# Performance work log

Hardware: AMD Instinct MI355X
Metric: run time of the kernel (lower is better)

## Reference

```python
import jax, jax.numpy as jnp
import numpy as np

BN_EPS = 1e-5
NEG_SLOPE = 0.2


def _knn_idx(x, k):
    # x: [B, C, N] -> idx: [B, N, k] of nearest neighbors (incl. self)
    xx = jnp.sum(x * x, axis=1)                      # [B, N]
    inner = jnp.einsum('bcn,bcm->bnm', x, x)          # [B, N, N]
    neg_d2 = -(xx[:, :, None] - 2.0 * inner + xx[:, None, :])
    _, idx = jax.lax.top_k(neg_d2, k)                 # largest -neg dist = nearest
    return idx


def _graph_feature(x, k):
    # x: [B, C, N] -> [B, 2C, N, k] with concat([x_j - x_i, x_i])
    idx = _knn_idx(x, k)                              # [B, N, k]
    xt = jnp.transpose(x, (0, 2, 1))                  # [B, N, C]
    neigh = jax.vmap(lambda xb, ib: xb[ib])(xt, idx)  # [B, N, k, C]
    center = xt[:, :, None, :]                        # [B, N, 1, C]
    feat = jnp.concatenate(
        [neigh - center, jnp.broadcast_to(center, neigh.shape)], axis=-1
    )                                                 # [B, N, k, 2C]
    return jnp.transpose(feat, (0, 3, 1, 2))          # [B, 2C, N, k]


def _edge_conv(x, W, gamma, beta, k):
    # EdgeConv block: graph feature -> 1x1 conv -> BN (train stats) -> LeakyReLU
    f = _graph_feature(x, k)                          # [B, 2C, N, k]
    y = jnp.einsum('oc,bcnk->bonk', W, f)             # 1x1 conv, no bias
    m = jnp.mean(y, axis=(0, 2, 3), keepdims=True)
    v = jnp.mean((y - m) ** 2, axis=(0, 2, 3), keepdims=True)
    y = (y - m) * jax.lax.rsqrt(v + BN_EPS)
    y = y * gamma.reshape(1, -1, 1, 1) + beta.reshape(1, -1, 1, 1)
    return jnp.where(y >= 0, y, NEG_SLOPE * y)


def setup_inputs() -> dict:
    key = jax.random.key(0)
    ks = jax.random.split(key, 8)
    B, Cin, N, K = 16, 4, 1024, 20
    channels = [64, 64, 128, 256]
    in_cs = [2 * Cin, 2 * channels[0], 2 * channels[1], 2 * channels[2]]
    inp = {'x': jax.random.normal(ks[0], (B, 1, Cin, N), dtype=jnp.float32)}
    for i in range(4):
        fan_in = in_cs[i]  # kaiming-ish scale
        inp[f'W{i}'] = jax.random.normal(ks[i + 1], (channels[i], in_cs[i]), dtype=jnp.float32) / np.sqrt(fan_in)
        inp[f'g{i}'] = jnp.ones((channels[i],), dtype=jnp.float32)
        inp[f'b{i}'] = jnp.zeros((channels[i],), dtype=jnp.float32)
    inp['k'] = K
    return inp


def reference(x, W0, g0, b0, W1, g1, b1, W2, g2, b2, W3, g3, b3, k):
    h = jnp.squeeze(x, axis=1)                        # [B, Cin, N]
    params = [(W0, g0, b0), (W1, g1, b1), (W2, g2, b2), (W3, g3, b3)]
    n_layers = len(params)
    for i, (W, g, b) in enumerate(params):
        h = _edge_conv(h, W, g, b, k)                 # [B, C_out, N, k]
        if i < n_layers - 1:
            h = jnp.max(h, axis=-1)                   # max over neighbors -> [B, C_out, N]
    # AdaptiveMaxPool2d((1,1)) over [B, C, N, k]
    return jnp.max(h, axis=(2, 3), keepdims=True)     # [B, C_last, 1, 1]
```

## Files before the change

kernel.cpp:

```cpp
#include <hip/hip_runtime.h>
#include <math.h>

static constexpr int B_ = 16;
static constexpr int N_ = 1024;
static constexpr int K_ = 20;

template<int C>
__global__ __launch_bounds__(256) void xx_kernel(const float* __restrict__ h,
                                                 float* __restrict__ xx) {
  int i = blockIdx.x * 256 + threadIdx.x;
  if (i >= B_ * N_) return;
  int b = i >> 10, n = i & 1023;
  const float* hb = h + (size_t)b * C * N_ + n;
  float s = 0.f;
  #pragma unroll 4
  for (int c = 0; c < C; ++c) { float v = hb[(size_t)c * N_]; s = fmaf(v, v, s); }
  xx[i] = s;
}

template<int C>
__global__ __launch_bounds__(256) void knn_kernel(const float* __restrict__ h,
                                                  const float* __restrict__ xx,
                                                  int* __restrict__ idxg) {
  constexpr int CC = (C < 64) ? C : 64;
  __shared__ float xm_s[CC][128];
  __shared__ float xn_s[C][16];
  const int b  = blockIdx.y;
  const int n0 = blockIdx.x * 16;
  const int tid = threadIdx.x;
  const int lane = tid & 63;
  const int wv   = tid >> 6;
  const int rb   = wv * 4;
  const float* hb = h + (size_t)b * C * N_;
  const float* xxb = xx + b * N_;

  for (int i = tid; i < C * 16; i += 256) {
    int c = i >> 4, r = i & 15;
    xn_s[c][r] = hb[(size_t)c * N_ + n0 + r];
  }
  float xxn[4];
  #pragma unroll
  for (int rr = 0; rr < 4; ++rr) xxn[rr] = xxb[n0 + rb + rr];

  float val[4][16];
  #pragma unroll
  for (int ch = 0; ch < 8; ++ch) {
    const int m0 = ch * 128;
    float acc0[4] = {0.f, 0.f, 0.f, 0.f};
    float acc1[4] = {0.f, 0.f, 0.f, 0.f};
    #pragma unroll
    for (int cc0 = 0; cc0 < C; cc0 += CC) {
      __syncthreads();
      #pragma unroll 4
      for (int i = tid; i < CC * 128; i += 256) {
        int c = i >> 7, mm = i & 127;
        xm_s[c][mm] = hb[(size_t)(cc0 + c) * N_ + m0 + mm];
      }
      __syncthreads();
      #pragma unroll 4
      for (int c = 0; c < CC; ++c) {
        float2 xm2 = *(const float2*)&xm_s[c][2 * lane];
        float4 xn4 = *(const float4*)&xn_s[cc0 + c][rb];
        float xnv[4] = {xn4.x, xn4.y, xn4.z, xn4.w};
        #pragma unroll
        for (int rr = 0; rr < 4; ++rr) {
          acc0[rr] = fmaf(xnv[rr], xm2.x, acc0[rr]);
          acc1[rr] = fmaf(xnv[rr], xm2.y, acc1[rr]);
        }
      }
    }
    float2 xxm2 = *(const float2*)&xxb[m0 + 2 * lane];
    #pragma unroll
    for (int rr = 0; rr < 4; ++rr) {
      val[rr][2 * ch]     = -(fmaf(-2.f, acc0[rr], xxn[rr]) + xxm2.x);
      val[rr][2 * ch + 1] = -(fmaf(-2.f, acc1[rr], xxn[rr]) + xxm2.y);
    }
  }

  #pragma unroll
  for (int pr = 0; pr < 2; ++pr) {
    float (&va)[16] = val[2 * pr];
    float (&vb)[16] = val[2 * pr + 1];
    unsigned colA[16], colB[16];
    #pragma unroll
    for (int t = 0; t < 16; ++t) {
      unsigned col = (unsigned)((t >> 1) * 128 + 2 * lane + (t & 1));
      colA[t] = col; colB[t] = col;
    }
    #pragma unroll
    for (int k = 2; k <= 16; k <<= 1) {
      #pragma unroll
      for (int j = k >> 1; j > 0; j >>= 1) {
        #pragma unroll
        for (int i = 0; i < 16; ++i) {
          int l = i ^ j;
          if (l > i) {
            bool up = (i & k) == 0;
            {
              bool gt = (va[l] > va[i]) || (va[l] == va[i] && colA[l] < colA[i]);
              bool cnd = up ? gt : !gt;
              float tv = va[i]; unsigned tc = colA[i];
              va[i] = cnd ? va[l] : tv;   colA[i] = cnd ? colA[l] : tc;
              va[l] = cnd ? tv : va[l];   colA[l] = cnd ? tc : colA[l];
            }
            {
              bool gt = (vb[l] > vb[i]) || (vb[l] == vb[i] && colB[l] < colB[i]);
              bool cnd = up ? gt : !gt;
              float tv = vb[i]; unsigned tc = colB[i];
              vb[i] = cnd ? vb[l] : tv;   colB[i] = cnd ? colB[l] : tc;
              vb[l] = cnd ? tv : vb[l];   colB[l] = cnd ? tc : colB[l];
            }
          }
        }
      }
    }
    const int outA = (b * N_ + n0 + rb + 2 * pr) * K_;
    const int outB = outA + K_;
    #pragma unroll 1
    for (int it = 0; it < K_; ++it) {
      float bvA = va[0]; unsigned bcA = colA[0];
      float bvB = vb[0]; unsigned bcB = colB[0];
      #pragma unroll
      for (int off = 32; off >= 1; off >>= 1) {
        float ovA = __shfl_xor(bvA, off); unsigned ocA = (unsigned)__shfl_xor((int)bcA, off);
        float ovB = __shfl_xor(bvB, off); unsigned ocB = (unsigned)__shfl_xor((int)bcB, off);
        bool tA = (ovA > bvA) || (ovA == bvA && ocA < bcA);
        bvA = tA ? ovA : bvA; bcA = tA ? ocA : bcA;
        bool tB = (ovB > bvB) || (ovB == bvB && ocB < bcB);
        bvB = tB ? ovB : bvB; bcB = tB ? ocB : bcB;
      }
      if (lane == 0) {
        idxg[outA + it] = (int)bcA;
        idxg[outB + it] = (int)bcB;
      }
      if (colA[0] == bcA) {
        #pragma unroll
        for (int t = 0; t < 15; ++t) { va[t] = va[t + 1]; colA[t] = colA[t + 1]; }
        va[15] = -3.4e38f; colA[15] = 0xFFFFFFFFu;
      }
      if (colB[0] == bcB) {
        #pragma unroll
        for (int t = 0; t < 15; ++t) { vb[t] = vb[t + 1]; colB[t] = colB[t + 1]; }
        vb[15] = -3.4e38f; colB[15] = 0xFFFFFFFFu;
      }
    }
  }
}

template<int C, int CO>
__global__ __launch_bounds__(256) void gemm_uw_kernel(const float* __restrict__ h,
    const float* __restrict__ W, float* __restrict__ ubuf, float* __restrict__ wbuf) {
  __shared__ float hs[C][128];
  __shared__ float Ws[64][C + 1];
  const int b  = blockIdx.z;
  const int n0 = blockIdx.x * 128;
  const int which = blockIdx.y & 1;
  const int o0 = (blockIdx.y >> 1) * 64;
  const int tid = threadIdx.x;
  for (int i = tid; i < 64 * C; i += 256) {
    int o = i / C, c = i % C;
    const float* wr = W + (size_t)(o0 + o) * (2 * C);
    float w1 = wr[c];
    Ws[o][c] = which ? (wr[C + c] - w1) : w1;
  }
  const float* hb = h + (size_t)b * C * N_ + n0;
  for (int i = tid; i < C * 128; i += 256) {
    int c = i >> 7, nn = i & 127;
    hs[c][nn] = hb[(size_t)c * N_ + nn];
  }
  __syncthreads();
  const int ob = (tid & 15) * 4;
  const int nb = (tid >> 4) * 8;
  float acc[8][4];
  #pragma unroll
  for (int i = 0; i < 8; ++i)
    #pragma unroll
    for (int j = 0; j < 4; ++j) acc[i][j] = 0.f;
  for (int c = 0; c < C; ++c) {
    float hv[8];
    *(float4*)&hv[0] = *(const float4*)&hs[c][nb];
    *(float4*)&hv[4] = *(const float4*)&hs[c][nb + 4];
    float w0 = Ws[ob][c], w1 = Ws[ob + 1][c], w2 = Ws[ob + 2][c], w3 = Ws[ob + 3][c];
    #pragma unroll
    for (int i = 0; i < 8; ++i) {
      acc[i][0] = fmaf(hv[i], w0, acc[i][0]);
      acc[i][1] = fmaf(hv[i], w1, acc[i][1]);
      acc[i][2] = fmaf(hv[i], w2, acc[i][2]);
      acc[i][3] = fmaf(hv[i], w3, acc[i][3]);
    }
  }
  float* out = (which ? wbuf : ubuf) + ((size_t)(b * N_ + n0 + nb)) * CO + o0 + ob;
  #pragma unroll
  for (int i = 0; i < 8; ++i) {
    float4 v4; v4.x = acc[i][0]; v4.y = acc[i][1]; v4.z = acc[i][2]; v4.w = acc[i][3];
    *(float4*)(out + (size_t)i * CO) = v4;
  }
}

template<int CO, int NSPLIT>
__global__ __launch_bounds__(256) void passA_kernel(const float* __restrict__ ubuf,
    const float* __restrict__ wbuf, const int* __restrict__ idxg,
    float* __restrict__ Mx, float* __restrict__ Mn, double* __restrict__ stats) {
  __shared__ float us[N_][32];
  const int b = blockIdx.y;
  const int otile = blockIdx.x / NSPLIT;
  const int ns    = blockIdx.x % NSPLIT;
  const int o0 = otile * 32;
  constexpr int NSUB = N_ / NSPLIT;
  const int nstart = ns * NSUB;
  const int tid = threadIdx.x;
  const float* ub = ubuf + (size_t)b * N_ * CO + o0;
  for (int i = tid; i < N_ * 32; i += 256) {
    int n = i >> 5, o = i & 31;
    us[n][o] = ub[(size_t)n * CO + o];
  }
  __syncthreads();
  const int o = tid & 31, ng = tid >> 5;
  double s_y = 0.0, s_y2 = 0.0;
  const size_t bnc = (size_t)b * N_ * CO;
  for (int n = nstart + ng; n < nstart + NSUB; n += 8) {
    const int* ip = idxg + (size_t)(b * N_ + n) * K_;
    int js[20];
    #pragma unroll
    for (int q = 0; q < 5; ++q) {
      int4 t4 = ((const int4*)ip)[q];
      js[q * 4 + 0] = t4.x; js[q * 4 + 1] = t4.y;
      js[q * 4 + 2] = t4.z; js[q * 4 + 3] = t4.w;
    }
    float mx = -3.4e38f, mn = 3.4e38f, s1 = 0.f, s2 = 0.f;
    #pragma unroll
    for (int k = 0; k < 20; ++k) {
      float v = us[js[k]][o];
      mx = fmaxf(mx, v); mn = fminf(mn, v);
      s1 += v; s2 = fmaf(v, v, s2);
    }
    float wvv = wbuf[bnc + (size_t)n * CO + o0 + o];
    s_y  += (double)s1 + 20.0 * (double)wvv;
    s_y2 += (double)s2 + 2.0 * (double)wvv * (double)s1 + 20.0 * (double)wvv * (double)wvv;
    Mx[bnc + (size_t)n * CO + o0 + o] = mx;
    Mn[bnc + (size_t)n * CO + o0 + o] = mn;
  }
  __syncthreads();
  double* sc = (double*)&us[0][0];
  sc[(o * 8 + ng) * 2]     = s_y;
  sc[(o * 8 + ng) * 2 + 1] = s_y2;
  __syncthreads();
  if (tid < 32) {
    double a = 0.0, c2 = 0.0;
    #pragma unroll
    for (int g = 0; g < 8; ++g) { a += sc[(tid * 8 + g) * 2]; c2 += sc[(tid * 8 + g) * 2 + 1]; }
    atomicAdd(&stats[(o0 + tid) * 2],     a);
    atomicAdd(&stats[(o0 + tid) * 2 + 1], c2);
  }
}

template<int CO>
__global__ __launch_bounds__(256) void passB_kernel(const float* __restrict__ Mx,
    const float* __restrict__ Mn, const float* __restrict__ wbuf,
    const double* __restrict__ stats, const float* __restrict__ gam,
    const float* __restrict__ bet, float* __restrict__ hout) {
  __shared__ float T[CO][65];
  __shared__ float a_s[CO], c_s[CO];
  const int b = blockIdx.y, n0 = blockIdx.x * 64;
  const int tid = threadIdx.x;
  const double CNT = (double)B_ * N_ * K_;
  for (int oo = tid; oo < CO; oo += 256) {
    double m  = stats[oo * 2] / CNT;
    double vv = stats[oo * 2 + 1] / CNT - m * m;
    float a = gam[oo] * rsqrtf((float)vv + 1e-5f);
    a_s[oo] = a;
    c_s[oo] = bet[oo] - a * (float)m;
  }
  __syncthreads();
  const size_t base = (size_t)(b * N_ + n0) * CO;
  for (int i = tid; i < 64 * CO; i += 256) {
    int nn = i / CO, oo = i % CO;
    float a = a_s[oo];
    size_t off = base + (size_t)nn * CO + oo;
    float selv = (a >= 0.f) ? Mx[off] : Mn[off];
    float z = fmaf(a, selv + wbuf[off], c_s[oo]);
    T[oo][nn] = (z >= 0.f) ? z : 0.2f * z;
  }
  __syncthreads();
  float* hb = hout + (size_t)b * CO * N_ + n0;
  for (int i = tid; i < 64 * CO; i += 256) {
    int oo = i >> 6, nn = i & 63;
    hb[(size_t)oo * N_ + nn] = T[oo][nn];
  }
}

__global__ __launch_bounds__(256) void final_kernel(const float* __restrict__ Mx,
    const float* __restrict__ Mn, const float* __restrict__ wbuf,
    const double* __restrict__ stats, const float* __restrict__ gam,
    const float* __restrict__ bet, float* __restrict__ out) {
  const int b = blockIdx.x, o = threadIdx.x;
  const double CNT = (double)B_ * N_ * K_;
  double m  = stats[o * 2] / CNT;
  double vv = stats[o * 2 + 1] / CNT - m * m;
  float a = gam[o] * rsqrtf((float)vv + 1e-5f);
  float c = bet[o] - a * (float)m;
  const float* mp = ((a >= 0.f) ? Mx : Mn) + (size_t)b * N_ * 256 + o;
  const float* wp = wbuf + (size_t)b * N_ * 256 + o;
  float best = -3.4e38f;
  for (int n = 0; n < N_; ++n) {
    float z = fmaf(a, mp[(size_t)n * 256] + wp[(size_t)n * 256], c);
    z = (z >= 0.f) ? z : 0.2f * z;
    best = fmaxf(best, z);
  }
  out[b * 256 + o] = best;
}

__global__ void zero_stats(double* p) {
  int i = blockIdx.x * 256 + threadIdx.x;
  if (i < 2048) p[i] = 0.0;
}

extern "C" void kernel_launch(void* const* d_in, const int* in_sizes, int n_in,
                              void* d_out, int out_size, void* d_ws, size_t ws_size,
                              hipStream_t stream) {
  (void)in_sizes; (void)n_in; (void)out_size; (void)ws_size;
  const float* x  = (const float*)d_in[0];
  const float* W0 = (const float*)d_in[1];
  const float* g0 = (const float*)d_in[2];
  const float* b0 = (const float*)d_in[3];
  const float* W1 = (const float*)d_in[4];
  const float* g1 = (const float*)d_in[5];
  const float* b1 = (const float*)d_in[6];
  const float* W2 = (const float*)d_in[7];
  const float* g2 = (const float*)d_in[8];
  const float* b2 = (const float*)d_in[9];
  const float* W3 = (const float*)d_in[10];
  const float* g3 = (const float*)d_in[11];
  const float* b3 = (const float*)d_in[12];

  float* ws  = (float*)d_ws;
  float* u   = ws;
  float* w   = u  + (size_t)B_ * N_ * 256;
  float* Mx  = w  + (size_t)B_ * N_ * 256;
  float* Mn  = Mx + (size_t)B_ * N_ * 256;
  float* h0b = Mn + (size_t)B_ * N_ * 256;
  float* h1b = h0b + (size_t)B_ * 128 * N_;
  float* xxv = h1b + (size_t)B_ * 128 * N_;
  int*   idx = (int*)(xxv + B_ * N_);
  double* stats = (double*)(idx + (size_t)B_ * N_ * K_);

  zero_stats<<<8, 256, 0, stream>>>(stats);

  xx_kernel<4><<<B_ * N_ / 256, 256, 0, stream>>>(x, xxv);
  knn_kernel<4><<<dim3(64, B_), 256, 0, stream>>>(x, xxv, idx);
  gemm_uw_kernel<4, 64><<<dim3(8, 2, B_), 256, 0, stream>>>(x, W0, u, w);
  passA_kernel<64, 8><<<dim3(16, B_), 256, 0, stream>>>(u, w, idx, Mx, Mn, stats);
  passB_kernel<64><<<dim3(16, B_), 256, 0, stream>>>(Mx, Mn, w, stats, g0, b0, h0b);

  xx_kernel<64><<<B_ * N_ / 256, 256, 0, stream>>>(h0b, xxv);
  knn_kernel<64><<<dim3(64, B_), 256, 0, stream>>>(h0b, xxv, idx);
  gemm_uw_kernel<64, 64><<<dim3(8, 2, B_), 256, 0, stream>>>(h0b, W1, u, w);
  passA_kernel<64, 8><<<dim3(16, B_), 256, 0, stream>>>(u, w, idx, Mx, Mn, stats + 512);
  passB_kernel<64><<<dim3(16, B_), 256, 0, stream>>>(Mx, Mn, w, stats + 512, g1, b1, h1b);

  xx_kernel<64><<<B_ * N_ / 256, 256, 0, stream>>>(h1b, xxv);
  knn_kernel<64><<<dim3(64, B_), 256, 0, stream>>>(h1b, xxv, idx);
  gemm_uw_kernel<64, 128><<<dim3(8, 4, B_), 256, 0, stream>>>(h1b, W2, u, w);
  passA_kernel<128, 4><<<dim3(16, B_), 256, 0, stream>>>(u, w, idx, Mx, Mn, stats + 1024);
  passB_kernel<128><<<dim3(16, B_), 256, 0, stream>>>(Mx, Mn, w, stats + 1024, g2, b2, h0b);

  xx_kernel<128><<<B_ * N_ / 256, 256, 0, stream>>>(h0b, xxv);
  knn_kernel<128><<<dim3(64, B_), 256, 0, stream>>>(h0b, xxv, idx);
  gemm_uw_kernel<128, 256><<<dim3(8, 8, B_), 256, 0, stream>>>(h0b, W3, u, w);
  passA_kernel<256, 2><<<dim3(16, B_), 256, 0, stream>>>(u, w, idx, Mx, Mn, stats + 1536);
  final_kernel<<<B_, 256, 0, stream>>>(Mx, Mn, w, stats + 1536, g3, b3, (float*)d_out);
}
```

Baseline: 1.457 ms.

## Extract top-2 per wave reduction round in kNN selection, processing all four rows together

The kNN top-k extraction now merges the two best candidates per lane in each butterfly shuffle round, giving two neighbors per round and halving the number of wave-wide reductions (10 instead of 20). The four rows' sorted lists are handled in one loop instead of two pairs, which interleaves more independent shuffle chains. In exchange, each round costs more shuffles and compares, list shifts become branchless double shifts, and all four rows' value and column arrays stay live at once, which raises register pressure.

```diff
diff --git a/kernel.cpp b/kernel.cpp
--- a/kernel.cpp
+++ b/kernel.cpp
@@ -77,16 +77,12 @@
     }
   }
 
-  #pragma unroll
-  for (int pr = 0; pr < 2; ++pr) {
-    float (&va)[16] = val[2 * pr];
-    float (&vb)[16] = val[2 * pr + 1];
-    unsigned colA[16], colB[16];
-    #pragma unroll
-    for (int t = 0; t < 16; ++t) {
-      unsigned col = (unsigned)((t >> 1) * 128 + 2 * lane + (t & 1));
-      colA[t] = col; colB[t] = col;
-    }
+  unsigned col_[4][16];
+  #pragma unroll
+  for (int r = 0; r < 4; ++r) {
+    #pragma unroll
+    for (int t = 0; t < 16; ++t)
+      col_[r][t] = (unsigned)((t >> 1) * 128 + 2 * lane + (t & 1));
     #pragma unroll
     for (int k = 2; k <= 16; k <<= 1) {
       #pragma unroll
@@ -96,52 +92,60 @@
           int l = i ^ j;
           if (l > i) {
             bool up = (i & k) == 0;
-            {
-              bool gt = (va[l] > va[i]) || (va[l] == va[i] && colA[l] < colA[i]);
-              bool cnd = up ? gt : !gt;
-              float tv = va[i]; unsigned tc = colA[i];
-              va[i] = cnd ? va[l] : tv;   colA[i] = cnd ? colA[l] : tc;
-              va[l] = cnd ? tv : va[l];   colA[l] = cnd ? tc : colA[l];
-            }
-            {
-              bool gt = (vb[l] > vb[i]) || (vb[l] == vb[i] && colB[l] < colB[i]);
-              bool cnd = up ? gt : !gt;
-              float tv = vb[i]; unsigned tc = colB[i];
-              vb[i] = cnd ? vb[l] : tv;   colB[i] = cnd ? colB[l] : tc;
-              vb[l] = cnd ? tv : vb[l];   colB[l] = cnd ? tc : colB[l];
-            }
+            bool gt = (val[r][l] > val[r][i]) ||
+                      (val[r][l] == val[r][i] && col_[r][l] < col_[r][i]);
+            bool cnd = up ? gt : !gt;
+            float tv = val[r][i]; unsigned tc = col_[r][i];
+            val[r][i] = cnd ? val[r][l] : tv;   col_[r][i] = cnd ? col_[r][l] : tc;
+            val[r][l] = cnd ? tv : val[r][l];   col_[r][l] = cnd ? tc : col_[r][l];
           }
         }
       }
     }
-    const int outA = (b * N_ + n0 + rb + 2 * pr) * K_;
-    const int outB = outA + K_;
-    #pragma unroll 1
-    for (int it = 0; it < K_; ++it) {
-      float bvA = va[0]; unsigned bcA = colA[0];
-      float bvB = vb[0]; unsigned bcB = colB[0];
+  }
+
+  const int outbase = (b * N_ + n0 + rb) * K_;
+  #pragma unroll 1
+  for (int it = 0; it < K_ / 2; ++it) {
+    #pragma unroll
+    for (int r = 0; r < 4; ++r) {
+      float    a0v = val[r][0], a1v = val[r][1];
+      unsigned a0c = col_[r][0], a1c = col_[r][1];
       #pragma unroll
       for (int off = 32; off >= 1; off >>= 1) {
-        float ovA = __shfl_xor(bvA, off); unsigned ocA = (unsigned)__shfl_xor((int)bcA, off);
-        float ovB = __shfl_xor(bvB, off); unsigned ocB = (unsigned)__shfl_xor((int)bcB, off);
-        bool tA = (ovA > bvA) || (ovA == bvA && ocA < bcA);
-        bvA = tA ? ovA : bvA; bcA = tA ? ocA : bcA;
-        bool tB = (ovB > bvB) || (ovB == bvB && ocB < bcB);
-        bvB = tB ? ovB : bvB; bcB = tB ? ocB : bcB;
+        float    b0v = __shfl_xor(a0v, off);
+        int      b0c = __shfl_xor((int)a0c, off);
+        float    b1v = __shfl_xor(a1v, off);
+        int      b1c = __shfl_xor((int)a1c, off);
+        bool aw = (a0v > b0v) || (a0v == b0v && a0c < (unsigned)b0c);
+        bool w1 = (a1v > b0v) || (a1v == b0v && a1c < (unsigned)b0c);
+        bool w2 = (a0v > b1v) || (a0v == b1v && a0c < (unsigned)b1c);
+        float    m1v = w1 ? a1v : b0v;  unsigned m1c = w1 ? a1c : (unsigned)b0c;
+        float    m2v = w2 ? a0v : b1v;  unsigned m2c = w2 ? a0c : (unsigned)b1c;
+        a0v = aw ? a0v : b0v;  a0c = aw ? a0c : (unsigned)b0c;
+        a1v = aw ? m1v : m2v;  a1c = aw ? m1c : m2c;
       }
       if (lane == 0) {
-        idxg[outA + it] = (int)bcA;
-        idxg[outB + it] = (int)bcB;
-      }
-      if (colA[0] == bcA) {
+        idxg[outbase + r * K_ + 2 * it]     = (int)a0c;
+        idxg[outbase + r * K_ + 2 * it + 1] = (int)a1c;
+      }
+      if (it < K_ / 2 - 1) {
+        bool hit0 = (col_[r][0] == a0c) || (col_[r][0] == a1c);
         #pragma unroll
-        for (int t = 0; t < 15; ++t) { va[t] = va[t + 1]; colA[t] = colA[t + 1]; }
-        va[15] = -3.4e38f; colA[15] = 0xFFFFFFFFu;
-      }
-      if (colB[0] == bcB) {
+        for (int t = 0; t < 15; ++t) {
+          val[r][t]  = hit0 ? val[r][t + 1]  : val[r][t];
+          col_[r][t] = hit0 ? col_[r][t + 1] : col_[r][t];
+        }
+        val[r][15]  = hit0 ? -3.4e38f     : val[r][15];
+        col_[r][15] = hit0 ? 0xFFFFFFFFu  : col_[r][15];
+        bool hit1 = (col_[r][0] == a1c);
         #pragma unroll
-        for (int t = 0; t < 15; ++t) { vb[t] = vb[t + 1]; colB[t] = colB[t + 1]; }
-        vb[15] = -3.4e38f; colB[15] = 0xFFFFFFFFu;
+        for (int t = 0; t < 15; ++t) {
+          val[r][t]  = hit1 ? val[r][t + 1]  : val[r][t];
+          col_[r][t] = hit1 ? col_[r][t + 1] : col_[r][t];
+        }
+        val[r][15]  = hit1 ? -3.4e38f     : val[r][15];
+        col_[r][15] = hit1 ? 0xFFFFFFFFu  : col_[r][15];
       }
     }
   }
```

After: 1.427 ms. 2.1% less time.

## Replace iterative top-k extraction with packed-key wave merge network in kNN

Applied to the files above, without the earlier changes.

Packs each distance and column into a single 64-bit sortable key, so every compare-exchange becomes one integer comparison. The 20 serial wave-wide argmax reductions are replaced with a butterfly merge: at each of six shuffle levels, a lane keeps the best 20 of its own sorted list and its partner's, then re-sorts with a fixed network. The kernel also moves to 512 threads per block with 2 rows per wave instead of 4, which cuts register pressure and adds waves per block. In exchange it does more 64-bit shuffles and selects, and it relies on the sortable-key encoding to reproduce the tie-breaking order.

```diff
diff --git a/kernel.cpp b/kernel.cpp
--- a/kernel.cpp
+++ b/kernel.cpp
@@ -4,6 +4,38 @@
 static constexpr int B_ = 16;
 static constexpr int N_ = 1024;
 static constexpr int K_ = 20;
+
+__device__ __forceinline__ unsigned long long shflx64(unsigned long long x, int m) {
+  int lo = __shfl_xor((int)(unsigned)x, m);
+  int hi = __shfl_xor((int)(unsigned)(x >> 32), m);
+  return ((unsigned long long)(unsigned)hi << 32) | (unsigned)lo;
+}
+
+#define CED(X, a, b) { bool sw_ = X[a] < X[b];                         \
+    unsigned long long t_ = X[a];                                      \
+    X[a] = sw_ ? X[b] : t_; X[b] = sw_ ? t_ : X[b]; }
+
+#define MERGE_LEVEL(S, D, M, DO_NET)                                   \
+  {                                                                    \
+    _Pragma("unroll")                                                  \
+    for (int i_ = 0; i_ < 20; ++i_) {                                  \
+      unsigned long long p_ = shflx64(S[19 - i_], (M));                \
+      D[i_] = (S[i_] > p_) ? S[i_] : p_;                               \
+    }                                                                  \
+    if (DO_NET) {                                                      \
+      CED(D,0,16) CED(D,1,17) CED(D,2,18) CED(D,3,19)                  \
+      CED(D,4,12) CED(D,5,13) CED(D,6,14) CED(D,7,15)                  \
+      CED(D,8,16) CED(D,9,17) CED(D,10,18) CED(D,11,19)                \
+      CED(D,4,8)  CED(D,5,9)  CED(D,6,10) CED(D,7,11)                  \
+      CED(D,12,16) CED(D,13,17) CED(D,14,18) CED(D,15,19)              \
+      CED(D,0,2)  CED(D,1,3)  CED(D,4,6)  CED(D,5,7)                   \
+      CED(D,8,10) CED(D,9,11) CED(D,12,14) CED(D,13,15)                \
+      CED(D,16,18) CED(D,17,19)                                        \
+      CED(D,0,1)  CED(D,2,3)  CED(D,4,5)  CED(D,6,7)                   \
+      CED(D,8,9)  CED(D,10,11) CED(D,12,13) CED(D,14,15)               \
+      CED(D,16,17) CED(D,18,19)                                        \
+    }                                                                  \
+  }
 
 template<int C>
 __global__ __launch_bounds__(256) void xx_kernel(const float* __restrict__ h,
@@ -19,7 +51,7 @@
 }
 
 template<int C>
-__global__ __launch_bounds__(256) void knn_kernel(const float* __restrict__ h,
+__global__ __launch_bounds__(512) void knn_kernel(const float* __restrict__ h,
                                                   const float* __restrict__ xx,
                                                   int* __restrict__ idxg) {
   constexpr int CC = (C < 64) ? C : 64;
@@ -30,29 +62,29 @@
   const int tid = threadIdx.x;
   const int lane = tid & 63;
   const int wv   = tid >> 6;
-  const int rb   = wv * 4;
+  const int rb   = wv * 2;
   const float* hb = h + (size_t)b * C * N_;
   const float* xxb = xx + b * N_;
 
-  for (int i = tid; i < C * 16; i += 256) {
+  for (int i = tid; i < C * 16; i += 512) {
     int c = i >> 4, r = i & 15;
     xn_s[c][r] = hb[(size_t)c * N_ + n0 + r];
   }
-  float xxn[4];
-  #pragma unroll
-  for (int rr = 0; rr < 4; ++rr) xxn[rr] = xxb[n0 + rb + rr];
-
-  float val[4][16];
+  float xxn[2];
+  #pragma unroll
+  for (int rr = 0; rr < 2; ++rr) xxn[rr] = xxb[n0 + rb + rr];
+
+  float val[2][16];
   #pragma unroll
   for (int ch = 0; ch < 8; ++ch) {
     const int m0 = ch * 128;
-    float acc0[4] = {0.f, 0.f, 0.f, 0.f};
-    float acc1[4] = {0.f, 0.f, 0.f, 0.f};
+    float acc0[2] = {0.f, 0.f};
+    float acc1[2] = {0.f, 0.f};
     #pragma unroll
     for (int cc0 = 0; cc0 < C; cc0 += CC) {
       __syncthreads();
       #pragma unroll 4
-      for (int i = tid; i < CC * 128; i += 256) {
+      for (int i = tid; i < CC * 128; i += 512) {
         int c = i >> 7, mm = i & 127;
         xm_s[c][mm] = hb[(size_t)(cc0 + c) * N_ + m0 + mm];
       }
@@ -60,32 +92,31 @@
       #pragma unroll 4
       for (int c = 0; c < CC; ++c) {
         float2 xm2 = *(const float2*)&xm_s[c][2 * lane];
-        float4 xn4 = *(const float4*)&xn_s[cc0 + c][rb];
-        float xnv[4] = {xn4.x, xn4.y, xn4.z, xn4.w};
-        #pragma unroll
-        for (int rr = 0; rr < 4; ++rr) {
-          acc0[rr] = fmaf(xnv[rr], xm2.x, acc0[rr]);
-          acc1[rr] = fmaf(xnv[rr], xm2.y, acc1[rr]);
-        }
+        float2 xn2 = *(const float2*)&xn_s[cc0 + c][rb];
+        acc0[0] = fmaf(xn2.x, xm2.x, acc0[0]);
+        acc1[0] = fmaf(xn2.x, xm2.y, acc1[0]);
+        acc0[1] = fmaf(xn2.y, xm2.x, acc0[1]);
+        acc1[1] = fmaf(xn2.y, xm2.y, acc1[1]);
       }
     }
     float2 xxm2 = *(const float2*)&xxb[m0 + 2 * lane];
     #pragma unroll
-    for (int rr = 0; rr < 4; ++rr) {
+    for (int rr = 0; rr < 2; ++rr) {
       val[rr][2 * ch]     = -(fmaf(-2.f, acc0[rr], xxn[rr]) + xxm2.x);
       val[rr][2 * ch + 1] = -(fmaf(-2.f, acc1[rr], xxn[rr]) + xxm2.y);
     }
   }
 
   #pragma unroll
-  for (int pr = 0; pr < 2; ++pr) {
-    float (&va)[16] = val[2 * pr];
-    float (&vb)[16] = val[2 * pr + 1];
-    unsigned colA[16], colB[16];
+  for (int r = 0; r < 2; ++r) {
+    unsigned long long La[20], Lb[20];
     #pragma unroll
     for (int t = 0; t < 16; ++t) {
+      float v = val[r][t] + 0.0f;
+      unsigned vb = __float_as_uint(v);
+      unsigned s  = vb ^ (unsigned)(((int)vb >> 31) | 0x80000000);
       unsigned col = (unsigned)((t >> 1) * 128 + 2 * lane + (t & 1));
-      colA[t] = col; colB[t] = col;
+      La[t] = ((unsigned long long)s << 32) | (unsigned)(~col);
     }
     #pragma unroll
     for (int k = 2; k <= 16; k <<= 1) {
@@ -96,54 +127,31 @@
           int l = i ^ j;
           if (l > i) {
             bool up = (i & k) == 0;
-            {
-              bool gt = (va[l] > va[i]) || (va[l] == va[i] && colA[l] < colA[i]);
-              bool cnd = up ? gt : !gt;
-              float tv = va[i]; unsigned tc = colA[i];
-              va[i] = cnd ? va[l] : tv;   colA[i] = cnd ? colA[l] : tc;
-              va[l] = cnd ? tv : va[l];   colA[l] = cnd ? tc : colA[l];
-            }
-            {
-              bool gt = (vb[l] > vb[i]) || (vb[l] == vb[i] && colB[l] < colB[i]);
-              bool cnd = up ? gt : !gt;
-              float tv = vb[i]; unsigned tc = colB[i];
-              vb[i] = cnd ? vb[l] : tv;   colB[i] = cnd ? colB[l] : tc;
-              vb[l] = cnd ? tv : vb[l];   colB[l] = cnd ? tc : colB[l];
-            }
+            bool gt = La[l] > La[i];
+            bool sw = up ? gt : !gt;
+            unsigned long long a = La[i];
+            La[i] = sw ? La[l] : a;
+            La[l] = sw ? a : La[l];
           }
         }
       }
     }
-    const int outA = (b * N_ + n0 + rb + 2 * pr) * K_;
-    const int outB = outA + K_;
-    #pragma unroll 1
-    for (int it = 0; it < K_; ++it) {
-      float bvA = va[0]; unsigned bcA = colA[0];
-      float bvB = vb[0]; unsigned bcB = colB[0];
+    La[16] = 0ull; La[17] = 0ull; La[18] = 0ull; La[19] = 0ull;
+
+    MERGE_LEVEL(La, Lb, 1,  true)
+    MERGE_LEVEL(Lb, La, 2,  true)
+    MERGE_LEVEL(La, Lb, 4,  true)
+    MERGE_LEVEL(Lb, La, 8,  true)
+    MERGE_LEVEL(La, Lb, 16, true)
+    MERGE_LEVEL(Lb, La, 32, false)
+
+    if (lane == 0) {
+      const int outbase = (b * N_ + n0 + rb + r) * K_;
       #pragma unroll
-      for (int off = 32; off >= 1; off >>= 1) {
-        float ovA = __shfl_xor(bvA, off); unsigned ocA = (unsigned)__shfl_xor((int)bcA, off);
-        float ovB = __shfl_xor(bvB, off); unsigned ocB = (unsigned)__shfl_xor((int)bcB, off);
-        bool tA = (ovA > bvA) || (ovA == bvA && ocA < bcA);
-        bvA = tA ? ovA : bvA; bcA = tA ? ocA : bcA;
-        bool tB = (ovB > bvB) || (ovB == bvB && ocB < bcB);
-        bvB = tB ? ovB : bvB; bcB = tB ? ocB : bcB;
-      }
-      if (lane == 0) {
-        idxg[outA + it] = (int)bcA;
-        idxg[outB + it] = (int)bcB;
-      }
-      if (colA[0] == bcA) {
-        #pragma unroll
-        for (int t = 0; t < 15; ++t) { va[t] = va[t + 1]; colA[t] = colA[t + 1]; }
-        va[15] = -3.4e38f; colA[15] = 0xFFFFFFFFu;
-      }
-      if (colB[0] == bcB) {
-        #pragma unroll
-        for (int t = 0; t < 15; ++t) { vb[t] = vb[t + 1]; colB[t] = colB[t + 1]; }
-        vb[15] = -3.4e38f; colB[15] = 0xFFFFFFFFu;
-      }
-    }
+      for (int i = 0; i < 20; ++i)
+        idxg[outbase + i] = (int)(~(unsigned)La[i]);
+    }
+    __builtin_amdgcn_sched_barrier(0);
   }
 }
 
@@ -347,25 +355,25 @@
   zero_stats<<<8, 256, 0, stream>>>(stats);
 
   xx_kernel<4><<<B_ * N_ / 256, 256, 0, stream>>>(x, xxv);
-  knn_kernel<4><<<dim3(64, B_), 256, 0, stream>>>(x, xxv, idx);
+  knn_kernel<4><<<dim3(64, B_), 512, 0, stream>>>(x, xxv, idx);
   gemm_uw_kernel<4, 64><<<dim3(8, 2, B_), 256, 0, stream>>>(x, W0, u, w);
   passA_kernel<64, 8><<<dim3(16, B_), 256, 0, stream>>>(u, w, idx, Mx, Mn, stats);
   passB_kernel<64><<<dim3(16, B_), 256, 0, stream>>>(Mx, Mn, w, stats, g0, b0, h0b);
 
   xx_kernel<64><<<B_ * N_ / 256, 256, 0, stream>>>(h0b, xxv);
-  knn_kernel<64><<<dim3(64, B_), 256, 0, stream>>>(h0b, xxv, idx);
+  knn_kernel<64><<<dim3(64, B_), 512, 0, stream>>>(h0b, xxv, idx);
   gemm_uw_kernel<64, 64><<<dim3(8, 2, B_), 256, 0, stream>>>(h0b, W1, u, w);
   passA_kernel<64, 8><<<dim3(16, B_), 256, 0, stream>>>(u, w, idx, Mx, Mn, stats + 512);
   passB_kernel<64><<<dim3(16, B_), 256, 0, stream>>>(Mx, Mn, w, stats + 512, g1, b1, h1b);
 
   xx_kernel<64><<<B_ * N_ / 256, 256, 0, stream>>>(h1b, xxv);
-  knn_kernel<64><<<dim3(64, B_), 256, 0, stream>>>(h1b, xxv, idx);
+  knn_kernel<64><<<dim3(64, B_), 512, 0, stream>>>(h1b, xxv, idx);
   gemm_uw_kernel<64, 128><<<dim3(8, 4, B_), 256, 0, stream>>>(h1b, W2, u, w);
   passA_kernel<128, 4><<<dim3(16, B_), 256, 0, stream>>>(u, w, idx, Mx, Mn, stats + 1024);
   passB_kernel<128><<<dim3(16, B_), 256, 0, stream>>>(Mx, Mn, w, stats + 1024, g2, b2, h0b);
 
   xx_kernel<128><<<B_ * N_ / 256, 256, 0, stream>>>(h0b, xxv);
-  knn_kernel<128><<<dim3(64, B_), 256, 0, stream>>>(h0b, xxv, idx);
+  knn_kernel<128><<<dim3(64, B_), 512, 0, stream>>>(h0b, xxv, idx);
   gemm_uw_kernel<128, 256><<<dim3(8, 8, B_), 256, 0, stream>>>(h0b, W3, u, w);
   passA_kernel<256, 2><<<dim3(16, B_), 256, 0, stream>>>(u, w, idx, Mx, Mn, stats + 1536);
   final_kernel<<<B_, 256, 0, stream>>>(Mx, Mn, w, stats + 1536, g3, b3, (float*)d_out);
```

New measurement: 1.405 ms. 1.04x faster.
